# Kernel optimization log

Measured on AMD Instinct MI355X. Metric: run time of the kernel, lower is better.

The kernel has to match this reference:

```python
import jax, jax.numpy as jnp
import numpy as np

B, S, H, NH = 2, 2048, 512, 8
DK = H // NH


def setup_inputs() -> dict:
    key = jax.random.key(0)
    ks = jax.random.split(key, 12)
    inp = {
        "query": jax.random.normal(ks[0], (B, S, H), dtype=jnp.float32),
        "key": jax.random.normal(ks[1], (B, S, H), dtype=jnp.float32),
        "value": jax.random.normal(ks[2], (B, S, H), dtype=jnp.float32),
        "bias": jax.random.normal(ks[3], (B, 1, S, S), dtype=jnp.float32),
        "mask": jax.random.randint(ks[4], (B, S), 0, 2, dtype=jnp.int32),
        "Wq": jax.random.normal(ks[5], (H, H), dtype=jnp.float32) * 0.02,
        "bq": jax.random.normal(ks[6], (H,), dtype=jnp.float32) * 0.02,
        "Wk": jax.random.normal(ks[7], (H, H), dtype=jnp.float32) * 0.02,
        "bk": jax.random.normal(ks[8], (H,), dtype=jnp.float32) * 0.02,
        "Wv": jax.random.normal(ks[9], (H, H), dtype=jnp.float32) * 0.02,
        "bv": jax.random.normal(ks[10], (H,), dtype=jnp.float32) * 0.02,
    }
    return inp


def reference(query, key, value, bias, mask, Wq, bq, Wk, bk, Wv, bv):
    b = query.shape[0]
    # torch nn.Linear: x @ W.T + b, then split heads -> [B, h, S, d_k]
    def proj(x, W, bb):
        y = x @ W.T + bb
        return y.reshape(b, -1, NH, DK).transpose(0, 2, 1, 3)

    q = proj(query, Wq, bq)
    k = proj(key, Wk, bk)
    v = proj(value, Wv, bv)

    score = jnp.einsum("bhqd,bhkd->bhqk", q, k) / np.sqrt(DK).astype(np.float32)
    # NOTE: the source swaps bias/mask when calling attention():
    #   the 0/1 mask is ADDED to the scores...
    mask_add = mask.reshape(b, 1, 1, -1).astype(score.dtype)
    score = score + mask_add
    #   ...and the float bias is used for the masked_fill (bias == 0 -> -1e30).
    score = jnp.where(bias == 0, jnp.asarray(-1e30, score.dtype), score)
    attn = jax.nn.softmax(score, axis=-1)  # dropout=None in the source call
    x = jnp.einsum("bhqk,bhkd->bhqd", attn, v)
    return x.transpose(0, 2, 1, 3).reshape(b, -1, NH * DK)
```

## Files before the change

kernel.cpp:

```cpp
#include <hip/hip_runtime.h>
#include <hip/hip_bf16.h>
#include <stdint.h>

#define B_  2
#define S_  2048
#define H_  512
#define NH_ 8
#define DK_ 64

typedef __bf16 bf16x8 __attribute__((ext_vector_type(8)));
typedef short  s16x4  __attribute__((ext_vector_type(4)));
typedef float  f32x4  __attribute__((ext_vector_type(4)));

static __device__ __forceinline__ uint32_t pk2(float a, float b) {
  __hip_bfloat162 h = __float22bfloat162_rn(float2{a, b});
  uint32_t u;
  __builtin_memcpy(&u, &h, 4);
  return u;
}

static __device__ __forceinline__ f32x4 mfma_k16(s16x4 a, s16x4 b, f32x4 c) {
#if defined(__HIP_DEVICE_COMPILE__)
  return __builtin_amdgcn_mfma_f32_16x16x16bf16_1k(a, b, c, 0, 0, 0);
#else
  (void)a; (void)b;
  return c;
#endif
}

typedef const __attribute__((address_space(1))) uint32_t* gas_t;
typedef __attribute__((address_space(3))) uint32_t* las_t;
static __device__ __forceinline__ void cp16(const void* g, void* l) {
  __builtin_amdgcn_global_load_lds((gas_t)g, (las_t)l, 16, 0, 0);
}

struct ProjArgs {
  const float* X[3];
  const float* W[3];
  const float* Bv[3];
  uint16_t*    O[3];
  const float* bias;
  const int*   mask;
  uint32_t*    zrow;
  float*       fmL;
};

__global__ __launch_bounds__(256) void prep_proj_kernel(ProjArgs pa) {
  __shared__ __align__(16) char psm[32768];
  int bid = blockIdx.x, t = threadIdx.x;

  if (bid >= 384) {
    if (bid < 896) {
      int rr = bid - 384;
      const float* base = pa.bias + (size_t)rr * 8 * 2048 + t * 8;
      uint4 a[8], b2[8];
#pragma unroll
      for (int i = 0; i < 8; i++) {
        const uint4* src = (const uint4*)(base + (size_t)i * 2048);
        a[i] = src[0]; b2[i] = src[1];
      }
      uint32_t (*wbuf)[4] = (uint32_t (*)[4])psm;
      int wv = t >> 6, ln = t & 63;
#pragma unroll
      for (int i = 0; i < 8; i++) {
        bool z = ((a[i].x << 1) == 0u) | ((a[i].y << 1) == 0u) |
                 ((a[i].z << 1) == 0u) | ((a[i].w << 1) == 0u) |
                 ((b2[i].x << 1) == 0u) | ((b2[i].y << 1) == 0u) |
                 ((b2[i].z << 1) == 0u) | ((b2[i].w << 1) == 0u);
        uint64_t m = __ballot(z);
        if (ln == 0) {
          uint32_t bits = 0;
#pragma unroll
          for (int c = 0; c < 8; c++)
            bits |= (uint32_t)(((m >> (8 * c)) & 0xFFull) != 0ull) << c;
          wbuf[i][wv] = bits;
        }
      }
      __syncthreads();
      if (t < 8)
        pa.zrow[rr * 8 + t] = wbuf[t][0] | (wbuf[t][1] << 8) |
                              (wbuf[t][2] << 16) | (wbuf[t][3] << 24);
    } else {
      const float LOG2E = 1.44269504088896340736f;
#pragma unroll
      for (int i = 0; i < 16; i++) {
        int idx = i * 256 + t;
        pa.fmL[idx] = (float)pa.mask[idx] * LOG2E;
      }
    }
    return;
  }

  int xcd = bid & 7, j = bid >> 3;
  int gi = ((j >> 2) << 3) | xcd;
  int dtile = j & 3;
  int mat = gi >> 5, mtile = gi & 31;
  int m0 = mtile * 128, n0 = dtile * 128;
  const float* X  = pa.X[mat];
  const float* Wt = pa.W[mat];
  const float* Bv = pa.Bv[mat];
  uint16_t*    O  = pa.O[mat];

  uint16_t (*Xs)[64] = (uint16_t (*)[64])psm;
  uint16_t (*Ws)[64] = (uint16_t (*)[64])(psm + 16384);

  int w = t >> 6, l = t & 63, lo = l & 15, g = l >> 4;
  int lr = l >> 4;
  int lc = l & 15;

  const float* Xp = X + (size_t)(m0 + w * 32 + lr) * 512 + lc * 4;
  const float* Wp = Wt + (size_t)(n0 + w * 32 + lr) * 512 + lc * 4;

  f32x4 acc[2][8];
#pragma unroll
  for (int st = 0; st < 2; st++)
#pragma unroll
    for (int dt = 0; dt < 8; dt++) acc[st][dt] = (f32x4){0.f, 0.f, 0.f, 0.f};

  float4 xa[8], wa2[8];
#pragma unroll
  for (int i = 0; i < 8; i++) xa[i] = *(const float4*)(Xp + (size_t)i * 4 * 512);
#pragma unroll
  for (int i = 0; i < 8; i++) wa2[i] = *(const float4*)(Wp + (size_t)i * 4 * 512);

  for (int kb = 0; kb < 8; kb++) {
#pragma unroll
    for (int i = 0; i < 8; i++) {
      int r = w * 32 + i * 4 + lr;
      int s0 = (lc >> 1) ^ (r & 7);
      uint2 pk{pk2(xa[i].x, xa[i].y), pk2(xa[i].z, xa[i].w)};
      *(uint2*)&Xs[r][s0 * 8 + (lc & 1) * 4] = pk;
    }
#pragma unroll
    for (int i = 0; i < 8; i++) {
      int r = w * 32 + i * 4 + lr;
      int s0 = (lc >> 1) ^ (r & 7);
      uint2 pk{pk2(wa2[i].x, wa2[i].y), pk2(wa2[i].z, wa2[i].w)};
      *(uint2*)&Ws[r][s0 * 8 + (lc & 1) * 4] = pk;
    }
    __syncthreads();
    if (kb < 7) {
      const float* Xn = Xp + (kb + 1) * 64;
      const float* Wn = Wp + (kb + 1) * 64;
#pragma unroll
      for (int i = 0; i < 8; i++) xa[i] = *(const float4*)(Xn + (size_t)i * 4 * 512);
#pragma unroll
      for (int i = 0; i < 8; i++) wa2[i] = *(const float4*)(Wn + (size_t)i * 4 * 512);
    }
#pragma unroll
    for (int kk = 0; kk < 2; kk++) {
      int seg = (kk * 4 + g) ^ (lo & 7);
      bf16x8 xf[2], wf[8];
#pragma unroll
      for (int st = 0; st < 2; st++)
        xf[st] = *(const bf16x8*)&Xs[w * 32 + st * 16 + lo][seg * 8];
#pragma unroll
      for (int dt = 0; dt < 8; dt++)
        wf[dt] = *(const bf16x8*)&Ws[dt * 16 + lo][seg * 8];
      if (mat < 2) {
#pragma unroll
        for (int st = 0; st < 2; st++)
#pragma unroll
          for (int dt = 0; dt < 8; dt++)
            acc[st][dt] = __builtin_amdgcn_mfma_f32_16x16x32_bf16(wf[dt], xf[st], acc[st][dt], 0, 0, 0);
      } else {
#pragma unroll
        for (int st = 0; st < 2; st++)
#pragma unroll
          for (int dt = 0; dt < 8; dt++)
            acc[st][dt] = __builtin_amdgcn_mfma_f32_16x16x32_bf16(xf[st], wf[dt], acc[st][dt], 0, 0, 0);
      }
    }
    __syncthreads();
  }

  if (mat < 2) {
    float scale = (mat == 0) ? 0.125f : 1.0f;
    float4 bv4[8];
#pragma unroll
    for (int dt = 0; dt < 8; dt++)
      bv4[dt] = *(const float4*)(Bv + n0 + dt * 16 + g * 4);
#pragma unroll
    for (int st = 0; st < 2; st++) {
      int ss = m0 + w * 32 + st * 16 + lo;
      int bb = ss >> 11, sIn = ss & 2047;
#pragma unroll
      for (int dt = 0; dt < 8; dt++) {
        int h2 = dtile * 2 + (dt >> 2);
        uint16_t* op = O + ((size_t)(bb * NH_ + h2) * S_ + sIn) * DK_ +
                       (dt & 3) * 16 + g * 4;
        float v0 = (acc[st][dt][0] + bv4[dt].x) * scale;
        float v1 = (acc[st][dt][1] + bv4[dt].y) * scale;
        float v2 = (acc[st][dt][2] + bv4[dt].z) * scale;
        float v3 = (acc[st][dt][3] + bv4[dt].w) * scale;
        uint2 pk{pk2(v0, v1), pk2(v2, v3)};
        *(uint2*)op = pk;
      }
    }
  } else {
    float bval[8];
#pragma unroll
    for (int dt = 0; dt < 8; dt++) bval[dt] = Bv[n0 + dt * 16 + lo];
#pragma unroll
    for (int st = 0; st < 2; st++) {
      int m = m0 + w * 32 + st * 16 + g * 4;
      int bb = m >> 11, sIn = m & 2047;
#pragma unroll
      for (int dt = 0; dt < 8; dt++) {
        int h2 = dtile * 2 + (dt >> 2);
        int dd = (dt & 3) * 16 + lo;
        float v0 = acc[st][dt][0] + bval[dt];
        float v1 = acc[st][dt][1] + bval[dt];
        float v2 = acc[st][dt][2] + bval[dt];
        float v3 = acc[st][dt][3] + bval[dt];
        uint2 pk{pk2(v0, v1), pk2(v2, v3)};
        *(uint2*)(O + ((size_t)(bb * NH_ + h2) * DK_ + dd) * S_ + sIn) = pk;
      }
    }
  }
}

__global__ __launch_bounds__(256) void attn_kernel(
    const uint16_t* __restrict__ Qb, const uint16_t* __restrict__ Kb,
    const uint16_t* __restrict__ Vt, const uint32_t* __restrict__ zrow,
    const float* __restrict__ fmL, const float* __restrict__ bias,
    float* __restrict__ out) {
  int bid = blockIdx.x;
  int bh = bid & 15, qtile = bid >> 4;
  int b = bh >> 3, h = bh & 7;
  int q0 = qtile * 64;
  int t = threadIdx.x;
  int w = t >> 6, l = t & 63, lo = l & 15, g = l >> 4;

  __shared__ __align__(16) char smem[32768];
  uint16_t* KsB = (uint16_t*)smem;
  uint16_t* VsB = (uint16_t*)(smem + 16384);

  const uint16_t* Qh = Qb + (size_t)bh * S_ * DK_;
  const uint16_t* Kh = Kb + (size_t)bh * S_ * DK_;
  const uint16_t* Vh = Vt + (size_t)bh * DK_ * S_;

  int lrow = l >> 3, lseg = (l & 7) ^ lrow;
  const uint16_t* kbase = Kh + (size_t)(w * 16 + lrow) * DK_ + lseg * 8;
  const uint16_t* vbase = Vh + (size_t)(w * 16 + lrow) * S_ + lseg * 8;
  uint16_t* kd0 = KsB + (w * 16) * 64;
  uint16_t* kd8 = KsB + (w * 16 + 8) * 64;
  uint16_t* vd0 = VsB + (w * 16) * 64;
  uint16_t* vd8 = VsB + (w * 16 + 8) * 64;

  uint32_t zall = zrow[(b << 11) + q0 + l];
#pragma unroll
  for (int s = 1; s < 64; s <<= 1) zall |= __shfl_xor(zall, s);

  bf16x8 qf[4][2];
#pragma unroll
  for (int qt = 0; qt < 4; qt++)
#pragma unroll
    for (int kk = 0; kk < 2; kk++)
      qf[qt][kk] = *(const bf16x8*)(Qh + (size_t)(q0 + qt * 16 + lo) * DK_ + kk * 32 + g * 8);

  f32x4 o[4][4];
#pragma unroll
  for (int dt = 0; dt < 4; dt++)
#pragma unroll
    for (int qt = 0; qt < 4; qt++) o[dt][qt] = (f32x4){0.f, 0.f, 0.f, 0.f};
  f32x4 tsa[4];
#pragma unroll
  for (int qt = 0; qt < 4; qt++) tsa[qt] = (f32x4){0.f, 0.f, 0.f, 0.f};
  const s16x4 vone = {(short)0x3F80, (short)0x3F80, (short)0x3F80, (short)0x3F80};

  const float* fmrow = fmL + b * S_ + w * 16 + g * 4;
  const float LOG2E = 1.44269504088896340736f;

  cp16(kbase, kd0);
  cp16(kbase + 512, kd8);
  cp16(vbase, vd0);
  cp16(vbase + 8 * S_, vd8);
  float4 mvc = *(const float4*)(fmrow);
  float4 mvn = mvc;

  for (int kb = 0; kb < 32; kb++) {
    int cur = kb & 1;
    int k0 = kb * 64;
    asm volatile("s_waitcnt vmcnt(0)" ::: "memory");
    __builtin_amdgcn_s_barrier();
    if (kb + 1 < 32) {
      int kn = k0 + 64;
      int nb = (cur ^ 1) * 4096;
      cp16(kbase + (size_t)kn * 64, kd0 + nb);
      cp16(kbase + (size_t)kn * 64 + 512, kd8 + nb);
      cp16(vbase + kn, vd0 + nb);
      cp16(vbase + kn + 8 * S_, vd8 + nb);
      mvn = *(const float4*)(fmrow + kn);
    }
    __builtin_amdgcn_sched_barrier(0);

    const uint16_t* KsT = KsB + cur * 4096;
    const uint16_t* VsT = VsB + cur * 4096;

    s16x4 vf[4];
    {
      int s = (2 * w + (g >> 1)) ^ (lo & 7);
      int off = s * 8 + (g & 1) * 4;
#pragma unroll
      for (int dt = 0; dt < 4; dt++)
        vf[dt] = *(const s16x4*)(VsT + (dt * 16 + lo) * 64 + off);
    }
    bf16x8 kf[2];
#pragma unroll
    for (int kk = 0; kk < 2; kk++) {
      int s = (kk * 4 + g) ^ (lo & 7);
      kf[kk] = *(const bf16x8*)(KsT + (w * 16 + lo) * 64 + s * 8);
    }

    f32x4 c[4];
#pragma unroll
    for (int qt = 0; qt < 4; qt++) {
      f32x4 z = {0.f, 0.f, 0.f, 0.f};
      z = __builtin_amdgcn_mfma_f32_16x16x32_bf16(kf[0], qf[qt][0], z, 0, 0, 0);
      c[qt] = __builtin_amdgcn_mfma_f32_16x16x32_bf16(kf[1], qf[qt][1], z, 0, 0, 0);
    }

    float4 mv4 = mvc;
    s16x4 pf[4];
    if (((zall >> kb) & 1u) == 0u) {
#pragma unroll
      for (int qt = 0; qt < 4; qt++) {
        float p0 = __builtin_amdgcn_exp2f(__builtin_fmaf(c[qt][0], LOG2E, mv4.x));
        float p1 = __builtin_amdgcn_exp2f(__builtin_fmaf(c[qt][1], LOG2E, mv4.y));
        float p2 = __builtin_amdgcn_exp2f(__builtin_fmaf(c[qt][2], LOG2E, mv4.z));
        float p3 = __builtin_amdgcn_exp2f(__builtin_fmaf(c[qt][3], LOG2E, mv4.w));
        union { s16x4 v; uint32_t u[2]; } uu;
        uu.u[0] = pk2(p0, p1);
        uu.u[1] = pk2(p2, p3);
        pf[qt] = uu.v;
      }
    } else {
#pragma unroll
      for (int qt = 0; qt < 4; qt++) {
        float4 bz = *(const float4*)(bias + ((size_t)(b * S_ + q0 + qt * 16 + lo)) * S_ + k0 + w * 16 + g * 4);
        float p0 = (bz.x == 0.f) ? 0.f : __builtin_amdgcn_exp2f(__builtin_fmaf(c[qt][0], LOG2E, mv4.x));
        float p1 = (bz.y == 0.f) ? 0.f : __builtin_amdgcn_exp2f(__builtin_fmaf(c[qt][1], LOG2E, mv4.y));
        float p2 = (bz.z == 0.f) ? 0.f : __builtin_amdgcn_exp2f(__builtin_fmaf(c[qt][2], LOG2E, mv4.z));
        float p3 = (bz.w == 0.f) ? 0.f : __builtin_amdgcn_exp2f(__builtin_fmaf(c[qt][3], LOG2E, mv4.w));
        union { s16x4 v; uint32_t u[2]; } uu;
        uu.u[0] = pk2(p0, p1);
        uu.u[1] = pk2(p2, p3);
        pf[qt] = uu.v;
      }
    }

#pragma unroll
    for (int qt = 0; qt < 4; qt++)
      tsa[qt] = mfma_k16(vone, pf[qt], tsa[qt]);

#pragma unroll
    for (int dt = 0; dt < 4; dt++)
#pragma unroll
      for (int qt = 0; qt < 4; qt++)
        o[dt][qt] = mfma_k16(vf[dt], pf[qt], o[dt][qt]);

    mvc = mvn;
  }

  float* OT = (float*)smem;
  float* LS = (float*)(smem + 8448);
  __syncthreads();
  if (g == 0) {
#pragma unroll
    for (int qt = 0; qt < 4; qt++) LS[(w * 4 + qt) * 16 + lo] = tsa[qt][0];
  }
#pragma unroll
  for (int qh = 0; qh < 2; qh++) {
#pragma unroll
    for (int ww = 0; ww < 4; ww++) {
      if (w == ww) {
#pragma unroll
        for (int dt = 0; dt < 4; dt++)
#pragma unroll
          for (int qt = 0; qt < 2; qt++)
#pragma unroll
            for (int r = 0; r < 4; r++) {
              int idx = (dt * 16 + g * 4 + r) * 33 + qt * 16 + lo;
              float val = o[dt][qh * 2 + qt][r];
              if (ww == 0) OT[idx] = val;
              else         OT[idx] += val;
            }
      }
      __syncthreads();
    }
    {
      int q = t >> 3, dseg = (t & 7) * 8;
      int qt2 = qh * 2 + (q >> 4), lo2 = q & 15;
      float lsum = LS[(0 * 4 + qt2) * 16 + lo2] + LS[(1 * 4 + qt2) * 16 + lo2] +
                   LS[(2 * 4 + qt2) * 16 + lo2] + LS[(3 * 4 + qt2) * 16 + lo2];
      float linv = 1.0f / fmaxf(lsum, 1e-30f);
      float* ob = out + ((size_t)(b * S_ + q0 + qh * 32 + q)) * H_ + h * DK_ + dseg;
#pragma unroll
      for (int i = 0; i < 2; i++) {
        float4 v;
        v.x = OT[(dseg + i * 4 + 0) * 33 + q] * linv;
        v.y = OT[(dseg + i * 4 + 1) * 33 + q] * linv;
        v.z = OT[(dseg + i * 4 + 2) * 33 + q] * linv;
        v.w = OT[(dseg + i * 4 + 3) * 33 + q] * linv;
        *(float4*)(ob + i * 4) = v;
      }
    }
    __syncthreads();
  }
}

extern "C" void kernel_launch(void* const* d_in, const int* in_sizes, int n_in,
                              void* d_out, int out_size, void* d_ws, size_t ws_size,
                              hipStream_t stream) {
  const float* query = (const float*)d_in[0];
  const float* key   = (const float*)d_in[1];
  const float* value = (const float*)d_in[2];
  const float* bias  = (const float*)d_in[3];
  const int*   mask  = (const int*)d_in[4];
  const float* Wq = (const float*)d_in[5];
  const float* bq = (const float*)d_in[6];
  const float* Wk = (const float*)d_in[7];
  const float* bk = (const float*)d_in[8];
  const float* Wv = (const float*)d_in[9];
  const float* bv = (const float*)d_in[10];

  char* ws = (char*)d_ws;
  uint32_t* zrow = (uint32_t*)ws;
  float*    fmL  = (float*)(ws + 16384);
  uint16_t* Qb = (uint16_t*)(ws + (size_t)(1 << 20));
  uint16_t* Kb = (uint16_t*)(ws + (size_t)(5 << 20));
  uint16_t* Vt = (uint16_t*)(ws + (size_t)(9 << 20));

  ProjArgs pa;
  pa.X[0] = query; pa.X[1] = key; pa.X[2] = value;
  pa.W[0] = Wq;    pa.W[1] = Wk;  pa.W[2] = Wv;
  pa.Bv[0] = bq;   pa.Bv[1] = bk; pa.Bv[2] = bv;
  pa.O[0] = Qb;    pa.O[1] = Kb;  pa.O[2] = Vt;
  pa.bias = bias;  pa.mask = mask;
  pa.zrow = zrow;  pa.fmL = fmL;

  prep_proj_kernel<<<897, 256, 0, stream>>>(pa);

  attn_kernel<<<512, 256, 0, stream>>>(Qb, Kb, Vt, zrow, fmL, bias, (float*)d_out);
}
```

Before: 160.4 us.

## Triple-buffer K/V tiles in LDS and stage mask row into shared memory

Replaces the double-buffered K/V async copy pipeline with a three-stage ring buffer. The loop now issues loads two tiles ahead and waits only for the older batch (vmcnt(4)) instead of draining all outstanding loads each iteration. The per-batch float mask row is also copied into LDS once up front rather than loaded from global memory per tile. The LDS footprint grows from 32 KB to 56 KB per block, which may reduce how many blocks fit per CU.

```diff
diff --git a/kernel.cpp b/kernel.cpp
--- a/kernel.cpp
+++ b/kernel.cpp
@@ -232,9 +232,7 @@
   int t = threadIdx.x;
   int w = t >> 6, l = t & 63, lo = l & 15, g = l >> 4;
 
-  __shared__ __align__(16) char smem[32768];
-  uint16_t* KsB = (uint16_t*)smem;
-  uint16_t* VsB = (uint16_t*)(smem + 16384);
+  __shared__ __align__(16) char smem[57344];
 
   const uint16_t* Qh = Qb + (size_t)bh * S_ * DK_;
   const uint16_t* Kh = Kb + (size_t)bh * S_ * DK_;
@@ -243,10 +241,24 @@
   int lrow = l >> 3, lseg = (l & 7) ^ lrow;
   const uint16_t* kbase = Kh + (size_t)(w * 16 + lrow) * DK_ + lseg * 8;
   const uint16_t* vbase = Vh + (size_t)(w * 16 + lrow) * S_ + lseg * 8;
-  uint16_t* kd0 = KsB + (w * 16) * 64;
-  uint16_t* kd8 = KsB + (w * 16 + 8) * 64;
-  uint16_t* vd0 = VsB + (w * 16) * 64;
-  uint16_t* vd8 = VsB + (w * 16 + 8) * 64;
+  int kdo = w * 2048;
+  int vdo = 8192 + w * 2048;
+
+  float* fmlds = (float*)(smem + 49152);
+  const float* fmG = fmL + b * S_;
+  cp16(fmG + w * 256 + l * 4, smem + 49152 + w * 1024);
+  cp16(fmG + 1024 + w * 256 + l * 4, smem + 49152 + 4096 + w * 1024);
+
+  auto stage = [&](const uint16_t* kp, const uint16_t* vp, uint32_t bufo) {
+    cp16(kp, smem + bufo + kdo);
+    cp16(kp + 512, smem + bufo + kdo + 1024);
+    cp16(vp, smem + bufo + vdo);
+    cp16(vp + 8 * S_, smem + bufo + vdo + 1024);
+  };
+  stage(kbase, vbase, 0);
+  stage(kbase + 4096, vbase + 64, 16384);
+  const uint16_t* kpS = kbase + 8192;
+  const uint16_t* vpS = vbase + 128;
 
   uint32_t zall = zrow[(b << 11) + q0 + l];
 #pragma unroll
@@ -269,34 +281,23 @@
   for (int qt = 0; qt < 4; qt++) tsa[qt] = (f32x4){0.f, 0.f, 0.f, 0.f};
   const s16x4 vone = {(short)0x3F80, (short)0x3F80, (short)0x3F80, (short)0x3F80};
 
-  const float* fmrow = fmL + b * S_ + w * 16 + g * 4;
   const float LOG2E = 1.44269504088896340736f;
 
-  cp16(kbase, kd0);
-  cp16(kbase + 512, kd8);
-  cp16(vbase, vd0);
-  cp16(vbase + 8 * S_, vd8);
-  float4 mvc = *(const float4*)(fmrow);
-  float4 mvn = mvc;
+  uint32_t oA = 0, oB = 16384, oC = 32768;
 
   for (int kb = 0; kb < 32; kb++) {
-    int cur = kb & 1;
     int k0 = kb * 64;
-    asm volatile("s_waitcnt vmcnt(0)" ::: "memory");
+    if (kb < 31) asm volatile("s_waitcnt vmcnt(4)" ::: "memory");
+    else         asm volatile("s_waitcnt vmcnt(0)" ::: "memory");
     __builtin_amdgcn_s_barrier();
-    if (kb + 1 < 32) {
-      int kn = k0 + 64;
-      int nb = (cur ^ 1) * 4096;
-      cp16(kbase + (size_t)kn * 64, kd0 + nb);
-      cp16(kbase + (size_t)kn * 64 + 512, kd8 + nb);
-      cp16(vbase + kn, vd0 + nb);
-      cp16(vbase + kn + 8 * S_, vd8 + nb);
-      mvn = *(const float4*)(fmrow + kn);
+    if (kb + 2 < 32) {
+      stage(kpS, vpS, oC);
+      kpS += 4096; vpS += 64;
     }
     __builtin_amdgcn_sched_barrier(0);
 
-    const uint16_t* KsT = KsB + cur * 4096;
-    const uint16_t* VsT = VsB + cur * 4096;
+    const uint16_t* KsT = (const uint16_t*)(smem + oA);
+    const uint16_t* VsT = (const uint16_t*)(smem + oA + 8192);
 
     s16x4 vf[4];
     {
@@ -321,7 +322,7 @@
       c[qt] = __builtin_amdgcn_mfma_f32_16x16x32_bf16(kf[1], qf[qt][1], z, 0, 0, 0);
     }
 
-    float4 mv4 = mvc;
+    float4 mv4 = *(const float4*)(fmlds + kb * 64 + w * 16 + g * 4);
     s16x4 pf[4];
     if (((zall >> kb) & 1u) == 0u) {
 #pragma unroll
@@ -360,7 +361,7 @@
       for (int qt = 0; qt < 4; qt++)
         o[dt][qt] = mfma_k16(vf[dt], pf[qt], o[dt][qt]);
 
-    mvc = mvn;
+    uint32_t tmp = oA; oA = oB; oB = oC; oC = tmp;
   }
 
   float* OT = (float*)smem;
```

Result: no change. 157.8 us (-1.6%).

## Stage 128-key blocks per barrier with larger LDS buffers and MFMA priority

Applied to the files above, without the earlier changes.

The attention loop now loads 128 keys per pipeline phase into a 64KB double-buffered shared memory region, halving the number of barriers and wait points, and processes two 64-key sub-blocks per phase. The V tile layout and swizzle change to match the wider stage, and s_setprio is raised around the MFMA sections so matrix work gets issue priority across waves. The mask row loads are no longer prefetched a step ahead but read inline. Doubling LDS usage per block may reduce occupancy.

```diff
diff --git a/kernel.cpp b/kernel.cpp
--- a/kernel.cpp
+++ b/kernel.cpp
@@ -232,21 +232,32 @@
   int t = threadIdx.x;
   int w = t >> 6, l = t & 63, lo = l & 15, g = l >> 4;
 
-  __shared__ __align__(16) char smem[32768];
-  uint16_t* KsB = (uint16_t*)smem;
-  uint16_t* VsB = (uint16_t*)(smem + 16384);
+  __shared__ __align__(16) char smem[65536];
 
   const uint16_t* Qh = Qb + (size_t)bh * S_ * DK_;
   const uint16_t* Kh = Kb + (size_t)bh * S_ * DK_;
   const uint16_t* Vh = Vt + (size_t)bh * DK_ * S_;
 
-  int lrow = l >> 3, lseg = (l & 7) ^ lrow;
-  const uint16_t* kbase = Kh + (size_t)(w * 16 + lrow) * DK_ + lseg * 8;
-  const uint16_t* vbase = Vh + (size_t)(w * 16 + lrow) * S_ + lseg * 8;
-  uint16_t* kd0 = KsB + (w * 16) * 64;
-  uint16_t* kd8 = KsB + (w * 16 + 8) * 64;
-  uint16_t* vd0 = VsB + (w * 16) * 64;
-  uint16_t* vd8 = VsB + (w * 16 + 8) * 64;
+  const uint16_t* kbase = Kh + (size_t)(w * 32 + (l >> 3)) * DK_ +
+                          ((l & 7) ^ (l >> 3)) * 8;
+  const uint16_t* vsrc[4];
+#pragma unroll
+  for (int i = 0; i < 4; i++) {
+    int vr = i * 4 + (l >> 4);
+    vsrc[i] = Vh + (size_t)(w * 16 + vr) * S_ + (((l & 15) ^ vr) * 8);
+  }
+
+  auto stage = [&](int ph, int buf) {
+    char* kb_ = smem + buf * 32768;
+    char* vb_ = smem + buf * 32768 + 16384;
+    const uint16_t* kp = kbase + (size_t)ph * 8192;
+#pragma unroll
+    for (int i = 0; i < 4; i++)
+      cp16(kp + (size_t)i * 8 * DK_, kb_ + (w * 32 + i * 8) * 128);
+#pragma unroll
+    for (int i = 0; i < 4; i++)
+      cp16(vsrc[i] + ph * 128, vb_ + (w * 16 + i * 4) * 256);
+  };
 
   uint32_t zall = zrow[(b << 11) + q0 + l];
 #pragma unroll
@@ -272,95 +283,90 @@
   const float* fmrow = fmL + b * S_ + w * 16 + g * 4;
   const float LOG2E = 1.44269504088896340736f;
 
-  cp16(kbase, kd0);
-  cp16(kbase + 512, kd8);
-  cp16(vbase, vd0);
-  cp16(vbase + 8 * S_, vd8);
-  float4 mvc = *(const float4*)(fmrow);
-  float4 mvn = mvc;
-
-  for (int kb = 0; kb < 32; kb++) {
-    int cur = kb & 1;
-    int k0 = kb * 64;
+  stage(0, 0);
+
+  for (int ph = 0; ph < 16; ph++) {
+    int buf = ph & 1;
     asm volatile("s_waitcnt vmcnt(0)" ::: "memory");
     __builtin_amdgcn_s_barrier();
-    if (kb + 1 < 32) {
-      int kn = k0 + 64;
-      int nb = (cur ^ 1) * 4096;
-      cp16(kbase + (size_t)kn * 64, kd0 + nb);
-      cp16(kbase + (size_t)kn * 64 + 512, kd8 + nb);
-      cp16(vbase + kn, vd0 + nb);
-      cp16(vbase + kn + 8 * S_, vd8 + nb);
-      mvn = *(const float4*)(fmrow + kn);
-    }
+    if (ph + 1 < 16) stage(ph + 1, buf ^ 1);
     __builtin_amdgcn_sched_barrier(0);
 
-    const uint16_t* KsT = KsB + cur * 4096;
-    const uint16_t* VsT = VsB + cur * 4096;
-
-    s16x4 vf[4];
-    {
-      int s = (2 * w + (g >> 1)) ^ (lo & 7);
-      int off = s * 8 + (g & 1) * 4;
+    const uint16_t* Ksb = (const uint16_t*)(smem + buf * 32768);
+    const uint16_t* Vsb = (const uint16_t*)(smem + buf * 32768 + 16384);
+
+#pragma unroll
+    for (int s0 = 0; s0 < 2; s0++) {
+      int kb64 = ph * 2 + s0;
+      int k0 = kb64 * 64;
+
+      s16x4 vf[4];
+      {
+        int sg = (s0 * 8 + w * 2 + (g >> 1));
+#pragma unroll
+        for (int dt = 0; dt < 4; dt++) {
+          int d = dt * 16 + lo;
+          vf[dt] = *(const s16x4*)((const char*)Vsb + d * 256 +
+                                   ((sg ^ lo) * 16) + (g & 1) * 8);
+        }
+      }
+      bf16x8 kf[2];
+#pragma unroll
+      for (int kk = 0; kk < 2; kk++) {
+        int sg = (kk * 4 + g) ^ (lo & 7);
+        kf[kk] = *(const bf16x8*)(Ksb + (s0 * 64 + w * 16 + lo) * 64 + sg * 8);
+      }
+
+      __builtin_amdgcn_s_setprio(1);
+      f32x4 c[4];
+#pragma unroll
+      for (int qt = 0; qt < 4; qt++) {
+        f32x4 z = {0.f, 0.f, 0.f, 0.f};
+        z = __builtin_amdgcn_mfma_f32_16x16x32_bf16(kf[0], qf[qt][0], z, 0, 0, 0);
+        c[qt] = __builtin_amdgcn_mfma_f32_16x16x32_bf16(kf[1], qf[qt][1], z, 0, 0, 0);
+      }
+      __builtin_amdgcn_s_setprio(0);
+
+      float4 mv4 = *(const float4*)(fmrow + k0);
+      s16x4 pf[4];
+      if (((zall >> kb64) & 1u) == 0u) {
+#pragma unroll
+        for (int qt = 0; qt < 4; qt++) {
+          float p0 = __builtin_amdgcn_exp2f(__builtin_fmaf(c[qt][0], LOG2E, mv4.x));
+          float p1 = __builtin_amdgcn_exp2f(__builtin_fmaf(c[qt][1], LOG2E, mv4.y));
+          float p2 = __builtin_amdgcn_exp2f(__builtin_fmaf(c[qt][2], LOG2E, mv4.z));
+          float p3 = __builtin_amdgcn_exp2f(__builtin_fmaf(c[qt][3], LOG2E, mv4.w));
+          union { s16x4 v; uint32_t u[2]; } uu;
+          uu.u[0] = pk2(p0, p1);
+          uu.u[1] = pk2(p2, p3);
+          pf[qt] = uu.v;
+        }
+      } else {
+#pragma unroll
+        for (int qt = 0; qt < 4; qt++) {
+          float4 bz = *(const float4*)(bias + ((size_t)(b * S_ + q0 + qt * 16 + lo)) * S_ + k0 + w * 16 + g * 4);
+          float p0 = (bz.x == 0.f) ? 0.f : __builtin_amdgcn_exp2f(__builtin_fmaf(c[qt][0], LOG2E, mv4.x));
+          float p1 = (bz.y == 0.f) ? 0.f : __builtin_amdgcn_exp2f(__builtin_fmaf(c[qt][1], LOG2E, mv4.y));
+          float p2 = (bz.z == 0.f) ? 0.f : __builtin_amdgcn_exp2f(__builtin_fmaf(c[qt][2], LOG2E, mv4.z));
+          float p3 = (bz.w == 0.f) ? 0.f : __builtin_amdgcn_exp2f(__builtin_fmaf(c[qt][3], LOG2E, mv4.w));
+          union { s16x4 v; uint32_t u[2]; } uu;
+          uu.u[0] = pk2(p0, p1);
+          uu.u[1] = pk2(p2, p3);
+          pf[qt] = uu.v;
+        }
+      }
+
+      __builtin_amdgcn_s_setprio(1);
+#pragma unroll
+      for (int qt = 0; qt < 4; qt++)
+        tsa[qt] = mfma_k16(vone, pf[qt], tsa[qt]);
 #pragma unroll
       for (int dt = 0; dt < 4; dt++)
-        vf[dt] = *(const s16x4*)(VsT + (dt * 16 + lo) * 64 + off);
-    }
-    bf16x8 kf[2];
-#pragma unroll
-    for (int kk = 0; kk < 2; kk++) {
-      int s = (kk * 4 + g) ^ (lo & 7);
-      kf[kk] = *(const bf16x8*)(KsT + (w * 16 + lo) * 64 + s * 8);
-    }
-
-    f32x4 c[4];
-#pragma unroll
-    for (int qt = 0; qt < 4; qt++) {
-      f32x4 z = {0.f, 0.f, 0.f, 0.f};
-      z = __builtin_amdgcn_mfma_f32_16x16x32_bf16(kf[0], qf[qt][0], z, 0, 0, 0);
-      c[qt] = __builtin_amdgcn_mfma_f32_16x16x32_bf16(kf[1], qf[qt][1], z, 0, 0, 0);
-    }
-
-    float4 mv4 = mvc;
-    s16x4 pf[4];
-    if (((zall >> kb) & 1u) == 0u) {
-#pragma unroll
-      for (int qt = 0; qt < 4; qt++) {
-        float p0 = __builtin_amdgcn_exp2f(__builtin_fmaf(c[qt][0], LOG2E, mv4.x));
-        float p1 = __builtin_amdgcn_exp2f(__builtin_fmaf(c[qt][1], LOG2E, mv4.y));
-        float p2 = __builtin_amdgcn_exp2f(__builtin_fmaf(c[qt][2], LOG2E, mv4.z));
-        float p3 = __builtin_amdgcn_exp2f(__builtin_fmaf(c[qt][3], LOG2E, mv4.w));
-        union { s16x4 v; uint32_t u[2]; } uu;
-        uu.u[0] = pk2(p0, p1);
-        uu.u[1] = pk2(p2, p3);
-        pf[qt] = uu.v;
-      }
-    } else {
-#pragma unroll
-      for (int qt = 0; qt < 4; qt++) {
-        float4 bz = *(const float4*)(bias + ((size_t)(b * S_ + q0 + qt * 16 + lo)) * S_ + k0 + w * 16 + g * 4);
-        float p0 = (bz.x == 0.f) ? 0.f : __builtin_amdgcn_exp2f(__builtin_fmaf(c[qt][0], LOG2E, mv4.x));
-        float p1 = (bz.y == 0.f) ? 0.f : __builtin_amdgcn_exp2f(__builtin_fmaf(c[qt][1], LOG2E, mv4.y));
-        float p2 = (bz.z == 0.f) ? 0.f : __builtin_amdgcn_exp2f(__builtin_fmaf(c[qt][2], LOG2E, mv4.z));
-        float p3 = (bz.w == 0.f) ? 0.f : __builtin_amdgcn_exp2f(__builtin_fmaf(c[qt][3], LOG2E, mv4.w));
-        union { s16x4 v; uint32_t u[2]; } uu;
-        uu.u[0] = pk2(p0, p1);
-        uu.u[1] = pk2(p2, p3);
-        pf[qt] = uu.v;
-      }
-    }
-
-#pragma unroll
-    for (int qt = 0; qt < 4; qt++)
-      tsa[qt] = mfma_k16(vone, pf[qt], tsa[qt]);
-
-#pragma unroll
-    for (int dt = 0; dt < 4; dt++)
-#pragma unroll
-      for (int qt = 0; qt < 4; qt++)
-        o[dt][qt] = mfma_k16(vf[dt], pf[qt], o[dt][qt]);
-
-    mvc = mvn;
+#pragma unroll
+        for (int qt = 0; qt < 4; qt++)
+          o[dt][qt] = mfma_k16(vf[dt], pf[qt], o[dt][qt]);
+      __builtin_amdgcn_s_setprio(0);
+    }
   }
 
   float* OT = (float*)smem;
```

New measurement: 165.6 us. 1.03x slower.
